# Performance work log

Hardware: AMD Instinct MI355X
Metric: run time of the kernel (lower is better)

The kernel has to match this reference:

```python
import jax, jax.numpy as jnp
import numpy as np
import math

D_HEAD = 64  # scaling uses sqrt(d_head), NOT sqrt of full projection dim (faithful to source)

def setup_inputs() -> dict:
    key = jax.random.key(0)
    ks = jax.random.split(key, 9)
    B, S, D = 4, 2048, 1024
    s = 0.02
    return {
        "x": jax.random.normal(ks[0], (B, S, D), dtype=jnp.float32),
        "Wq": jax.random.normal(ks[1], (D, D), dtype=jnp.float32) * s,
        "bq": jax.random.normal(ks[2], (D,), dtype=jnp.float32) * s,
        "Wk": jax.random.normal(ks[3], (D, D), dtype=jnp.float32) * s,
        "bk": jax.random.normal(ks[4], (D,), dtype=jnp.float32) * s,
        "Wv": jax.random.normal(ks[5], (D, D), dtype=jnp.float32) * s,
        "bv": jax.random.normal(ks[6], (D,), dtype=jnp.float32) * s,
        "Wo": jax.random.normal(ks[7], (D, D), dtype=jnp.float32) * s,
        "bo": jax.random.normal(ks[8], (D,), dtype=jnp.float32) * s,
    }

def reference(x, Wq, bq, Wk, bk, Wv, bv, Wo, bo):
    # Q/K/V projections: [B,S,D] @ [D,D] + b
    Q = jnp.einsum('bsd,de->bse', x, Wq) + bq
    K = jnp.einsum('bsd,de->bse', x, Wk) + bk
    V = jnp.einsum('bsd,de->bse', x, Wv) + bv
    # NOTE: source does bmm over the FULL projected dim (no head split),
    # scaled by sqrt(d_head) only.
    scores = jnp.einsum('bqd,bkd->bqk', Q, K) / math.sqrt(D_HEAD)  # [B,S,S]
    S_len = scores.shape[-1]
    causal = jnp.tril(jnp.ones((S_len, S_len), dtype=bool))
    scores = jnp.where(causal, scores, -jnp.inf)
    weights = jax.nn.softmax(scores, axis=-1)
    attn_out = jnp.einsum('bqk,bkd->bqd', weights, V)
    return jnp.einsum('bsd,de->bse', attn_out, Wo) + bo
```

## Files before the change

### kernel.cpp

```cpp
#include <hip/hip_runtime.h>
#include <stdint.h>

typedef _Float16 f16;
typedef __attribute__((ext_vector_type(8))) _Float16 f16x8;
typedef __attribute__((ext_vector_type(4))) _Float16 f16x4;
typedef __attribute__((ext_vector_type(4))) float f32x4;

#define BK 32

typedef __attribute__((address_space(3))) uint32_t lds_u32;
typedef const __attribute__((address_space(1))) uint32_t glb_u32;

__device__ __forceinline__ void gload_lds16(const void* g, void* l) {
    __builtin_amdgcn_global_load_lds((glb_u32*)g, (lds_u32*)l, 16, 0, 0);
}

template<int OUT_MODE, int CAUSAL, int TM, int TN>
__device__ __forceinline__
void gemm_body(const f16* __restrict__ A, const f16* __restrict__ B,
               const float* __restrict__ bias, const float* __restrict__ bias2,
               void* __restrict__ Cv, void* __restrict__ C2,
               int M, int N, int K,
               long long sAb, long long sBb, long long sCb, float scale,
               int bx, int by, int bzi)
{
    constexpr int IM = TM / 32;
    constexpr int JN = TN / 32;

    int mtile, n0;
    if (CAUSAL == 1) {
        int rem = bx, mi = 0;
        while (rem > mi) { rem -= mi + 1; ++mi; }
        mtile = mi;
        n0 = rem * TN;
    } else {
        mtile = by;
        n0 = bx * TN;
    }

    const int tid  = threadIdx.x;
    const int wave = tid >> 6;
    const int lane = tid & 63;
    const long long bz = bzi;
    A += bz * sAb;
    B += bz * sBb;

    __shared__ f16 As[TM * BK];
    __shared__ f16 Bs[TN * BK];

    const int srow  = lane >> 2;
    const int scolS = (((lane & 3) ^ ((srow >> 1) & 3))) * 8;
    const int fr    = lane & 15;
    const int fkS   = (((lane >> 4) ^ ((fr >> 1) & 3))) * 8;

    const int wm = (wave >> 1) * (TM / 2);
    const int wn = (wave & 1) * (TN / 2);

    const int npass = (CAUSAL == 2) ? 2 : 1;
    for (int pass = 0; pass < npass; ++pass) {
        const int mt = (CAUSAL == 2 && pass == 1) ? (M / TM - 1 - mtile) : mtile;
        const int m0 = mt * TM;
        const int Kend = (CAUSAL == 2) ? (m0 + TM) : K;

        f32x4 acc[IM][JN] = {};

        for (int k0 = 0; k0 < Kend; k0 += BK) {
            #pragma unroll
            for (int gg = 0; gg < TM / 64; ++gg) {
                const int g = wave * (TM / 64) + gg;
                gload_lds16(A + (long long)(m0 + g * 16 + srow) * K + (k0 + scolS),
                            &As[g * 512]);
            }
            #pragma unroll
            for (int gg = 0; gg < TN / 64; ++gg) {
                const int g = wave * (TN / 64) + gg;
                gload_lds16(B + (long long)(n0 + g * 16 + srow) * K + (k0 + scolS),
                            &Bs[g * 512]);
            }
            __syncthreads();

            f16x8 af[IM], bf[JN];
            #pragma unroll
            for (int i = 0; i < IM; ++i)
                af[i] = *(const f16x8*)&As[(wm + i * 16 + fr) * BK + fkS];
            #pragma unroll
            for (int j = 0; j < JN; ++j)
                bf[j] = *(const f16x8*)&Bs[(wn + j * 16 + fr) * BK + fkS];

            #pragma unroll
            for (int i = 0; i < IM; ++i)
                #pragma unroll
                for (int j = 0; j < JN; ++j)
                    acc[i][j] = __builtin_amdgcn_mfma_f32_16x16x32_f16(af[i], bf[j], acc[i][j], 0, 0, 0);
            __syncthreads();
        }

        const int cn = lane & 15;
        const int cm = (lane >> 4) * 4;
        #pragma unroll
        for (int j = 0; j < JN; ++j) {
            const int gn = n0 + wn + j * 16 + cn;
            #pragma unroll
            for (int i = 0; i < IM; ++i) {
                const int gm = m0 + wm + i * 16 + cm;
                if (OUT_MODE == 0) {
                    const float bv = bias ? bias[gn] : 0.f;
                    float* C = (float*)Cv + bz * sCb;
                    #pragma unroll
                    for (int r = 0; r < 4; ++r)
                        C[(long long)(gm + r) * N + gn] = acc[i][j][r] * scale + bv;
                } else if (OUT_MODE == 1) {
                    const float bv = bias ? bias[(long long)bz * N + gn] : 0.f;
                    f16* C = (f16*)Cv + bz * sCb;
                    #pragma unroll
                    for (int r = 0; r < 4; ++r)
                        C[(long long)(gm + r) * N + gn] = (f16)(acc[i][j][r] * scale + bv);
                } else {
                    const int sel = gn >> 10;
                    const int nn  = gn & 1023;
                    if (sel == 0) {
                        f16* C = (f16*)Cv;
                        #pragma unroll
                        for (int r = 0; r < 4; ++r)
                            C[(long long)(gm + r) * 1024 + nn] = (f16)acc[i][j][r];
                    } else {
                        const float bb = bias2[nn];
                        f16* C = (f16*)C2;
                        const int b = gm >> 11, s = gm & 2047;
                        f16x4 pk;
                        #pragma unroll
                        for (int r = 0; r < 4; ++r)
                            pk[r] = (f16)(acc[i][j][r] + bb);
                        *(f16x4*)&C[(long long)b * 2097152 + (long long)nn * 2048 + s] = pk;
                    }
                }
            }
        }
        if (CAUSAL == 2) __syncthreads();
    }
}

template<int OUT_MODE, int CAUSAL, int TM, int TN>
__global__ __launch_bounds__(256, 2)
void gemm_bt(const f16* __restrict__ A, const f16* __restrict__ B,
             const float* __restrict__ bias, const float* __restrict__ bias2,
             void* __restrict__ Cv, void* __restrict__ C2,
             int M, int N, int K,
             long long sAb, long long sBb, long long sCb, float scale)
{
    gemm_body<OUT_MODE, CAUSAL, TM, TN>(A, B, bias, bias2, Cv, C2, M, N, K,
                                        sAb, sBb, sCb, scale,
                                        blockIdx.x, blockIdx.y, blockIdx.z);
}


__device__ __forceinline__
void stage_half(const f16* __restrict__ G, int ldg, f16* lds_half,
                int grow0, int k0, int tid)
{
    const int lr  = tid >> 3;
    const int csw = ((tid & 7) * 8) ^ ((lr & 7) << 3);
    gload_lds16(G + (long long)(grow0 + lr) * ldg + (k0 + csw),
                lds_half + ((tid >> 6) << 9));
    gload_lds16(G + (long long)(grow0 + 64 + lr) * ldg + (k0 + csw),
                lds_half + 4096 + ((tid >> 6) << 9));
}

__global__ __launch_bounds__(512, 2)
void gemm_proj_8ph(const f16* __restrict__ A, const f16* __restrict__ B,
                   const float* __restrict__ bvo,
                   f16* __restrict__ Qh, f16* __restrict__ Vt,
                   int M, int N, int K)
{
    (void)M;
    __shared__ f16 As[2][16384];
    __shared__ f16 Bs[2][16384];

    const int nwg  = gridDim.x;
    const int orig = blockIdx.x;
    const int swz  = (orig & 7) * (nwg >> 3) + (orig >> 3);
    const int ntn  = N >> 8;
    const int mt = swz / ntn, nt = swz - mt * ntn;
    const int m0 = mt << 8, n0 = nt << 8;

    const int tid  = threadIdx.x;
    const int lane = tid & 63;
    const int wave = tid >> 6;
    const int wm = (wave >> 2) << 7;
    const int wn = (wave & 3) << 6;
    const int fr  = lane & 15;
    const int hk  = lane >> 4;
    const int lsw = lane & 7;
    const int nkt = K >> 6;

    f32x4 acc[8][4] = {};
    f16x8 bf[4][2];

    stage_half(A, K, &As[0][0],    m0,       0, tid);
    stage_half(A, K, &As[0][8192], m0 + 128, 0, tid);
    stage_half(B, K, &Bs[0][0],    n0,       0, tid);
    stage_half(B, K, &Bs[0][8192], n0 + 128, 0, tid);
    if (nkt > 1) {
        stage_half(B, K, &Bs[1][0],    n0,       64, tid);
        stage_half(B, K, &Bs[1][8192], n0 + 128, 64, tid);
        asm volatile("s_waitcnt vmcnt(4)" ::: "memory");
    } else {
        asm volatile("s_waitcnt vmcnt(0)" ::: "memory");
    }
    __builtin_amdgcn_s_barrier();

    for (int t = 0; t < nkt; ++t) {
        const f16* Ab = As[t & 1];
        const f16* Bb = Bs[t & 1];
        #pragma unroll
        for (int p = 0; p < 4; ++p) {
            if (p == 0) {
                #pragma unroll
                for (int j = 0; j < 4; ++j)
                    #pragma unroll
                    for (int kk = 0; kk < 2; ++kk)
                        bf[j][kk] = *(const f16x8*)((const char*)Bb +
                            ((wn + j * 16 + fr) << 7) +
                            ((((kk << 2) | hk) ^ lsw) << 4));
            }
            f16x8 af[2][2];
            #pragma unroll
            for (int ii = 0; ii < 2; ++ii)
                #pragma unroll
                for (int kk = 0; kk < 2; ++kk)
                    af[ii][kk] = *(const f16x8*)((const char*)Ab +
                        ((wm + (2 * p + ii) * 16 + fr) << 7) +
                        ((((kk << 2) | hk) ^ lsw) << 4));

            if (p == 0 && t + 1 < nkt)
                stage_half(A, K, &As[(t + 1) & 1][0],    m0,       (t + 1) << 6, tid);
            if (p == 1 && t + 1 < nkt)
                stage_half(A, K, &As[(t + 1) & 1][8192], m0 + 128, (t + 1) << 6, tid);
            if (p == 2 && t + 2 < nkt)
                stage_half(B, K, &Bs[t & 1][0],          n0,       (t + 2) << 6, tid);
            if (p == 3 && t + 2 < nkt)
                stage_half(B, K, &Bs[t & 1][8192],       n0 + 128, (t + 2) << 6, tid);

            if (p == 0) asm volatile("s_waitcnt lgkmcnt(8)" ::: "memory");
            __builtin_amdgcn_s_barrier();
            asm volatile("s_waitcnt lgkmcnt(0)" ::: "memory");
            __builtin_amdgcn_s_setprio(1);
            #pragma unroll
            for (int ii = 0; ii < 2; ++ii)
                #pragma unroll
                for (int j = 0; j < 4; ++j)
                    #pragma unroll
                    for (int kk = 0; kk < 2; ++kk)
                        acc[2 * p + ii][j] = __builtin_amdgcn_mfma_f32_16x16x32_f16(
                            af[ii][kk], bf[j][kk], acc[2 * p + ii][j], 0, 0, 0);
            __builtin_amdgcn_s_setprio(0);
            if (p == 3) {
                if (t + 2 < nkt) asm volatile("s_waitcnt vmcnt(4)" ::: "memory");
                else             asm volatile("s_waitcnt vmcnt(0)" ::: "memory");
            }
            __builtin_amdgcn_s_barrier();
        }
    }

    const int cn  = lane & 15;
    const int cm4 = (lane >> 4) * 4;
    #pragma unroll
    for (int j = 0; j < 4; ++j) {
        const int gn  = n0 + wn + j * 16 + cn;
        const int sel = gn >> 10;
        const int nn  = gn & 1023;
        #pragma unroll
        for (int i = 0; i < 8; ++i) {
            const int gm = m0 + wm + i * 16 + cm4;
            if (sel == 0) {
                #pragma unroll
                for (int r = 0; r < 4; ++r)
                    Qh[(long long)(gm + r) * 1024 + nn] = (f16)acc[i][j][r];
            } else {
                const float bb = bvo[nn];
                const int b = gm >> 11, s = gm & 2047;
                f16x4 pk;
                #pragma unroll
                for (int r = 0; r < 4; ++r)
                    pk[r] = (f16)(acc[i][j][r] + bb);
                *(f16x4*)&Vt[(long long)b * 2097152 + (long long)nn * 2048 + s] = pk;
            }
        }
    }
}

__global__ __launch_bounds__(256)
void prep(const float* __restrict__ x,  const float* __restrict__ Wq,
          const float* __restrict__ bq, const float* __restrict__ Wk,
          const float* __restrict__ Wv, const float* __restrict__ bv,
          const float* __restrict__ Wo,
          f16* __restrict__ xb,  f16* __restrict__ Wqf, f16* __restrict__ Wkf,
          f16* __restrict__ Wvf, f16* __restrict__ Wot,
          float* __restrict__ bvo, float* __restrict__ wvec)
{
    __shared__ f16 tile[32][33];
    __shared__ float red[4][64];
    const int t = threadIdx.x;
    int id = blockIdx.x;

    if (id < 8192) {
        const int i = (id * 256 + t) * 4;
        const float4 v = *(const float4*)&x[i];
        f16x4 o; o[0]=(f16)v.x; o[1]=(f16)v.y; o[2]=(f16)v.z; o[3]=(f16)v.w;
        *(f16x4*)&xb[i] = o;
        return;
    }
    id -= 8192;
    if (id < 3072) {
        const float* src = (id < 1024) ? Wq : (id < 2048) ? Wk : Wv;
        f16* dst = (id < 1024) ? Wqf : (id < 2048) ? Wkf : Wvf;
        const int i = ((id & 1023) * 256 + t) * 4;
        const float4 v = *(const float4*)&src[i];
        f16x4 o; o[0]=(f16)v.x; o[1]=(f16)v.y; o[2]=(f16)v.z; o[3]=(f16)v.w;
        *(f16x4*)&dst[i] = o;
        return;
    }
    id -= 3072;
    if (id < 1024) {
        const int bx = (id & 31) * 32, by = (id >> 5) * 32;
        const int tx = t & 31, ty = t >> 5;
        #pragma unroll
        for (int i = 0; i < 32; i += 8)
            tile[ty + i][tx] = (f16)Wo[(long long)(by + ty + i) * 1024 + (bx + tx)];
        __syncthreads();
        #pragma unroll
        for (int i = 0; i < 32; i += 8)
            Wot[(long long)(bx + ty + i) * 1024 + (by + tx)] = tile[tx][ty + i];
        return;
    }
    id -= 1024;
    if (id < 16) {
        const int e0 = id * 64;
        const int wave = t >> 6, lane = t & 63;
        float acc = 0.f;
        for (int i = 0; i < 256; ++i) {
            const int k = wave * 256 + i;
            acc += bv[k] * Wo[(long long)k * 1024 + e0 + lane];
        }
        red[wave][lane] = acc;
        __syncthreads();
        if (wave == 0)
            bvo[e0 + lane] = red[0][lane] + red[1][lane] + red[2][lane] + red[3][lane];
        return;
    }
    id -= 16;
    {
        const int row = id * 4 + (t >> 6);
        const int lane = t & 63;
        const float* src = Wk + (long long)row * 1024;
        float a = 0.f;
        #pragma unroll
        for (int tt = 0; tt < 16; ++tt) a += src[lane + 64 * tt] * bq[lane + 64 * tt];
        #pragma unroll
        for (int o = 32; o > 0; o >>= 1) a += __shfl_down(a, o);
        if (lane == 0) wvec[row] = a * 0.125f;
    }
}

__global__ __launch_bounds__(256, 2)
void dual_weights_cvec(const f16* __restrict__ Wkf, const f16* __restrict__ Wqf,
                       const f16* __restrict__ Wot, const f16* __restrict__ Wvf,
                       f16* __restrict__ Wcat2,
                       const f16* __restrict__ xb, const float* __restrict__ wvec,
                       float* __restrict__ cbias)
{
    if (blockIdx.z == 2) {
        const int flat = blockIdx.y * 16 + blockIdx.x;
        const int wave = threadIdx.x >> 6, lane = threadIdx.x & 63;
        #pragma unroll
        for (int rr = 0; rr < 8; ++rr) {
            const int row = (flat * 4 + wave) * 8 + rr;
            const f16* src = xb + (long long)row * 1024;
            float a = 0.f;
            #pragma unroll
            for (int tt = 0; tt < 16; ++tt)
                a += (float)src[lane + 64 * tt] * wvec[lane + 64 * tt];
            #pragma unroll
            for (int o = 32; o > 0; o >>= 1) a += __shfl_down(a, o);
            if (lane == 0) cbias[row] = a;
        }
        return;
    }
    const f16* Ax = (blockIdx.z == 0) ? Wkf : Wot;
    const f16* Bx = (blockIdx.z == 0) ? Wqf : Wvf;
    f16* Cx = Wcat2 + (long long)blockIdx.z * 1024 * 1024;
    gemm_body<1, 0, 64, 64>(Ax, Bx, nullptr, nullptr, Cx, nullptr,
                            1024, 1024, 1024, 0, 0, 0, 1.f,
                            blockIdx.x, blockIdx.y, 0);
}

__global__ __launch_bounds__(256)
void softmax_causal(const f16* __restrict__ Sc, f16* __restrict__ P, int S)
{
    const long long row = blockIdx.x;
    const int q = (int)(row % S);
    const f16* src = Sc + row * S;
    f16* dst = P + row * S;
    const int t = threadIdx.x;
    __shared__ float redm[4], reds[4];

    f16x8 vv = {};
    if (t * 8 <= q) vv = *(const f16x8*)&src[t * 8];
    float v[8];
    float mx = -3.0e38f;
    #pragma unroll
    for (int i = 0; i < 8; ++i) {
        const int k = t * 8 + i;
        v[i] = (float)vv[i];
        if (k <= q) mx = fmaxf(mx, v[i]);
    }
    #pragma unroll
    for (int o = 32; o > 0; o >>= 1) mx = fmaxf(mx, __shfl_down(mx, o));
    if ((t & 63) == 0) redm[t >> 6] = mx;
    __syncthreads();
    mx = fmaxf(fmaxf(redm[0], redm[1]), fmaxf(redm[2], redm[3]));

    float sum = 0.f;
    #pragma unroll
    for (int i = 0; i < 8; ++i) {
        const int k = t * 8 + i;
        v[i] = (k <= q) ? __expf(v[i] - mx) : 0.f;
        sum += v[i];
    }
    #pragma unroll
    for (int o = 32; o > 0; o >>= 1) sum += __shfl_down(sum, o);
    if ((t & 63) == 0) reds[t >> 6] = sum;
    __syncthreads();
    sum = reds[0] + reds[1] + reds[2] + reds[3];
    const float inv = 1.f / sum;
    f16x8 ov;
    #pragma unroll
    for (int i = 0; i < 8; ++i) ov[i] = (f16)(v[i] * inv);
    *(f16x8*)&dst[t * 8] = ov;
}

extern "C" void kernel_launch(void* const* d_in, const int* in_sizes, int n_in,
                              void* d_out, int out_size, void* d_ws, size_t ws_size,
                              hipStream_t stream)
{
    const float* x  = (const float*)d_in[0];
    const float* Wq = (const float*)d_in[1];
    const float* bq = (const float*)d_in[2];
    const float* Wk = (const float*)d_in[3];
    const float* Wv = (const float*)d_in[5];
    const float* bv = (const float*)d_in[6];
    const float* Wo = (const float*)d_in[7];
    const float* bo = (const float*)d_in[8];
    float* out = (float*)d_out;

    const int B = 4, S = 2048, D = 1024;
    const long long SD  = (long long)S * D;
    const long long SS  = (long long)S * S;
    const long long BSD = (long long)B * SD;
    const int MS = B * S;

    char* p = (char*)d_ws;
    f16*   xb    = (f16*)p;  p += BSD * 2;
    f16*   Wqf   = (f16*)p;  p += (long long)D * D * 2;
    f16*   Wkf   = (f16*)p;  p += (long long)D * D * 2;
    f16*   Wvf   = (f16*)p;  p += (long long)D * D * 2;
    f16*   Wot   = (f16*)p;  p += (long long)D * D * 2;
    f16*   Wcat2 = (f16*)p;  p += 2LL * D * D * 2;
    float* bvo   = (float*)p; p += D * 4;
    float* wvec  = (float*)p; p += D * 4;
    float* cbias = (float*)p; p += (long long)MS * 4;
    f16*   Qh    = (f16*)p;  p += BSD * 2;
    f16*   Vt    = (f16*)p;  p += BSD * 2;
    f16*   Sc    = (f16*)p;  p += (long long)B * SS * 2;
    f16*   Pb    = (f16*)p;  p += (long long)B * SS * 2;

    dim3 blk(256);

    prep<<<dim3(12560), blk, 0, stream>>>(x, Wq, bq, Wk, Wv, bv, Wo,
                                          xb, Wqf, Wkf, Wvf, Wot, bvo, wvec);

    dual_weights_cvec<<<dim3(16, 16, 3), blk, 0, stream>>>(Wkf, Wqf, Wot, Wvf,
                                                           Wcat2, xb, wvec, cbias);

    dim3 gproj((MS / 256) * (2 * D / 256));
    gemm_proj_8ph<<<gproj, dim3(512), 0, stream>>>(xb, Wcat2, bvo, Qh, Vt,
                                                   MS, 2 * D, D);

    dim3 gsc(136, 1, B);
    gemm_bt<1, 1, 128, 128><<<gsc, blk, 0, stream>>>(Qh, xb, cbias, nullptr,
                                                     Sc, nullptr,
                                                     S, S, D, SD, SD, SS, 0.125f);

    softmax_causal<<<dim3((unsigned)(B * S)), blk, 0, stream>>>(Sc, Pb, S);

    dim3 gpv(D / 64, S / 128 / 2, B);
    gemm_bt<0, 2, 128, 64><<<gpv, blk, 0, stream>>>(Pb, Vt, bo, nullptr,
                                                    out, nullptr,
                                                    S, D, S, SS, SD, SD, 1.f);
}
```

Before: 269.2 us.

## Add double-buffered BK=64 GEMM with direct-to-LDS loads for scores and PV

Introduces a new gemm2 kernel for the score GEMM and the PV GEMM. It uses double-buffered LDS tiles with a K-step of 64, XOR-swizzled global-to-LDS loads and prefetch of the next tile while MFMAs run on the current one, plus s_setprio around the MFMA block. The old path waited on each stage. This aims to hide global load latency and halve barrier count per K, at the cost of doubled LDS use (64KB for 128x128 tiles), which may reduce occupancy.

```diff
diff --git a/kernel.cpp b/kernel.cpp
--- a/kernel.cpp
+++ b/kernel.cpp
@@ -109,50 +109,163 @@
                     #pragma unroll
                     for (int r = 0; r < 4; ++r)
                         C[(long long)(gm + r) * N + gn] = acc[i][j][r] * scale + bv;
-                } else if (OUT_MODE == 1) {
+                } else {
                     const float bv = bias ? bias[(long long)bz * N + gn] : 0.f;
                     f16* C = (f16*)Cv + bz * sCb;
                     #pragma unroll
                     for (int r = 0; r < 4; ++r)
                         C[(long long)(gm + r) * N + gn] = (f16)(acc[i][j][r] * scale + bv);
+                }
+            }
+        }
+        if (CAUSAL == 2) __syncthreads();
+    }
+}
+
+
+template<int ROWS>
+__device__ __forceinline__
+void stage2(const f16* __restrict__ G, int ldg, f16* lds,
+            int grow0, int k0, int tid)
+{
+    const int l = tid & 63, w = tid >> 6;
+    #pragma unroll
+    for (int q = 0; q < ROWS / 32; ++q) {
+        const int r = q * 32 + w * 8 + (l >> 3);
+        const int csw = (((l & 7) ^ (r & 7)) << 3);
+        gload_lds16(G + (long long)(grow0 + r) * ldg + (k0 + csw),
+                    lds + q * 2048 + w * 512);
+    }
+}
+
+template<int OUT_MODE, int CAUSAL, int TM, int TN>
+__device__ __forceinline__
+void gemm2_body(const f16* __restrict__ A, const f16* __restrict__ B,
+                const float* __restrict__ bias, void* __restrict__ Cv,
+                int M, int N, int K,
+                long long sAb, long long sBb, long long sCb, float scale,
+                int bx, int by, int bzi)
+{
+    constexpr int IM = TM / 32;
+    constexpr int JN = TN / 32;
+
+    int mtile, n0;
+    if (CAUSAL == 1) {
+        int rem = bx, mi = 0;
+        while (rem > mi) { rem -= mi + 1; ++mi; }
+        mtile = mi;
+        n0 = rem * TN;
+    } else {
+        mtile = by;
+        n0 = bx * TN;
+    }
+
+    const int tid  = threadIdx.x;
+    const int wave = tid >> 6;
+    const int lane = tid & 63;
+    const long long bz = bzi;
+    A += bz * sAb;
+    B += bz * sBb;
+
+    __shared__ f16 As[2][TM * 64];
+    __shared__ f16 Bs[2][TN * 64];
+
+    const int fr  = lane & 15;
+    const int hk  = lane >> 4;
+    const int lsw = lane & 7;
+    const int wm  = (wave >> 1) * (TM / 2);
+    const int wn  = (wave & 1) * (TN / 2);
+
+    const int npass = (CAUSAL == 2) ? 2 : 1;
+    for (int pass = 0; pass < npass; ++pass) {
+        const int mt = (CAUSAL == 2 && pass == 1) ? (M / TM - 1 - mtile) : mtile;
+        const int m0 = mt * TM;
+        const int Kend = (CAUSAL == 2) ? (m0 + TM) : K;
+
+        f32x4 acc[IM][JN] = {};
+
+        stage2<TM>(A, K, &As[0][0], m0, 0, tid);
+        stage2<TN>(B, K, &Bs[0][0], n0, 0, tid);
+        asm volatile("s_waitcnt vmcnt(0)" ::: "memory");
+        __builtin_amdgcn_s_barrier();
+
+        int cur = 0;
+        for (int k0 = 0; k0 < Kend; k0 += 64) {
+            if (k0 + 64 < Kend) {
+                stage2<TM>(A, K, &As[cur ^ 1][0], m0, k0 + 64, tid);
+                stage2<TN>(B, K, &Bs[cur ^ 1][0], n0, k0 + 64, tid);
+            }
+
+            f16x8 af[IM][2], bf[JN][2];
+            #pragma unroll
+            for (int i = 0; i < IM; ++i)
+                #pragma unroll
+                for (int kk = 0; kk < 2; ++kk)
+                    af[i][kk] = *(const f16x8*)((const char*)&As[cur][0] +
+                        ((wm + i * 16 + fr) << 7) +
+                        ((((kk << 2) | hk) ^ lsw) << 4));
+            #pragma unroll
+            for (int j = 0; j < JN; ++j)
+                #pragma unroll
+                for (int kk = 0; kk < 2; ++kk)
+                    bf[j][kk] = *(const f16x8*)((const char*)&Bs[cur][0] +
+                        ((wn + j * 16 + fr) << 7) +
+                        ((((kk << 2) | hk) ^ lsw) << 4));
+
+            asm volatile("s_waitcnt lgkmcnt(0)" ::: "memory");
+            __builtin_amdgcn_s_setprio(1);
+            #pragma unroll
+            for (int i = 0; i < IM; ++i)
+                #pragma unroll
+                for (int j = 0; j < JN; ++j)
+                    #pragma unroll
+                    for (int kk = 0; kk < 2; ++kk)
+                        acc[i][j] = __builtin_amdgcn_mfma_f32_16x16x32_f16(
+                            af[i][kk], bf[j][kk], acc[i][j], 0, 0, 0);
+            __builtin_amdgcn_s_setprio(0);
+
+            asm volatile("s_waitcnt vmcnt(0)" ::: "memory");
+            __builtin_amdgcn_s_barrier();
+            cur ^= 1;
+        }
+
+        const int cn = lane & 15;
+        const int cm = (lane >> 4) * 4;
+        #pragma unroll
+        for (int j = 0; j < JN; ++j) {
+            const int gn = n0 + wn + j * 16 + cn;
+            #pragma unroll
+            for (int i = 0; i < IM; ++i) {
+                const int gm = m0 + wm + i * 16 + cm;
+                if (OUT_MODE == 0) {
+                    const float bv = bias ? bias[gn] : 0.f;
+                    float* C = (float*)Cv + bz * sCb;
+                    #pragma unroll
+                    for (int r = 0; r < 4; ++r)
+                        C[(long long)(gm + r) * N + gn] = acc[i][j][r] * scale + bv;
                 } else {
-                    const int sel = gn >> 10;
-                    const int nn  = gn & 1023;
-                    if (sel == 0) {
-                        f16* C = (f16*)Cv;
-                        #pragma unroll
-                        for (int r = 0; r < 4; ++r)
-                            C[(long long)(gm + r) * 1024 + nn] = (f16)acc[i][j][r];
-                    } else {
-                        const float bb = bias2[nn];
-                        f16* C = (f16*)C2;
-                        const int b = gm >> 11, s = gm & 2047;
-                        f16x4 pk;
-                        #pragma unroll
-                        for (int r = 0; r < 4; ++r)
-                            pk[r] = (f16)(acc[i][j][r] + bb);
-                        *(f16x4*)&C[(long long)b * 2097152 + (long long)nn * 2048 + s] = pk;
-                    }
+                    const float bv = bias ? bias[(long long)bz * N + gn] : 0.f;
+                    f16* C = (f16*)Cv + bz * sCb;
+                    #pragma unroll
+                    for (int r = 0; r < 4; ++r)
+                        C[(long long)(gm + r) * N + gn] = (f16)(acc[i][j][r] * scale + bv);
                 }
             }
         }
-        if (CAUSAL == 2) __syncthreads();
     }
 }
 
 template<int OUT_MODE, int CAUSAL, int TM, int TN>
 __global__ __launch_bounds__(256, 2)
-void gemm_bt(const f16* __restrict__ A, const f16* __restrict__ B,
-             const float* __restrict__ bias, const float* __restrict__ bias2,
-             void* __restrict__ Cv, void* __restrict__ C2,
-             int M, int N, int K,
-             long long sAb, long long sBb, long long sCb, float scale)
-{
-    gemm_body<OUT_MODE, CAUSAL, TM, TN>(A, B, bias, bias2, Cv, C2, M, N, K,
-                                        sAb, sBb, sCb, scale,
-                                        blockIdx.x, blockIdx.y, blockIdx.z);
-}
-
+void gemm2_bt(const f16* __restrict__ A, const f16* __restrict__ B,
+              const float* __restrict__ bias, void* __restrict__ Cv,
+              int M, int N, int K,
+              long long sAb, long long sBb, long long sCb, float scale)
+{
+    gemm2_body<OUT_MODE, CAUSAL, TM, TN>(A, B, bias, Cv, M, N, K,
+                                         sAb, sBb, sCb, scale,
+                                         blockIdx.x, blockIdx.y, blockIdx.z);
+}
 
 __device__ __forceinline__
 void stage_half(const f16* __restrict__ G, int ldg, f16* lds_half,
@@ -487,14 +600,12 @@
                                                    MS, 2 * D, D);
 
     dim3 gsc(136, 1, B);
-    gemm_bt<1, 1, 128, 128><<<gsc, blk, 0, stream>>>(Qh, xb, cbias, nullptr,
-                                                     Sc, nullptr,
-                                                     S, S, D, SD, SD, SS, 0.125f);
+    gemm2_bt<1, 1, 128, 128><<<gsc, blk, 0, stream>>>(Qh, xb, cbias, Sc,
+                                                      S, S, D, SD, SD, SS, 0.125f);
 
     softmax_causal<<<dim3((unsigned)(B * S)), blk, 0, stream>>>(Sc, Pb, S);
 
     dim3 gpv(D / 64, S / 128 / 2, B);
-    gemm_bt<0, 2, 128, 64><<<gpv, blk, 0, stream>>>(Pb, Vt, bo, nullptr,
-                                                    out, nullptr,
-                                                    S, D, S, SS, SD, SD, 1.f);
-}
+    gemm2_bt<0, 2, 128, 64><<<gpv, blk, 0, stream>>>(Pb, Vt, bo, out,
+                                                     S, D, S, SS, SD, SD, 1.f);
+}
```

After: 269.7 us. Within noise of the previous version (+0.2%).
